# Kernel tuning notes

Hardware: AMD Instinct MI355X
Metric: run time of the kernel (lower is better)

Reference implementation:

```python
import jax, jax.numpy as jnp
import numpy as np

PATCH_SIZE = 8
STRIDE = 4

def setup_inputs() -> dict:
    key = jax.random.key(0)
    k_x, k_w1, k_b1, k_w2, k_b2 = jax.random.split(key, 5)
    B, L, C = 8, 2048, 256
    X = jax.random.normal(k_x, (B, L, C), dtype=jnp.float32)
    # Conv1d(1, 64, patch_size) weight [64,1,ps] -> [64, ps]; Conv1d(64,2,1) -> [2,64]
    s1 = 1.0 / np.sqrt(PATCH_SIZE)
    s2 = 1.0 / np.sqrt(64.0)
    W1 = jax.random.uniform(k_w1, (64, PATCH_SIZE), jnp.float32, -s1, s1)
    b1 = jax.random.uniform(k_b1, (64,), jnp.float32, -s1, s1)
    W2 = jax.random.uniform(k_w2, (2, 64), jnp.float32, -s2, s2)
    b2 = jax.random.uniform(k_b2, (2,), jnp.float32, -s2, s2)
    return {"X": X, "W1": W1, "b1": b1, "W2": W2, "b2": b2}

def reference(X, W1, b1, W2, b2):
    B, L, C = X.shape
    ps, stride = PATCH_SIZE, STRIDE
    patch_count = (L - ps) // stride + 1  # 511
    # gather indices for sliding windows along sequence dim
    idx = jnp.arange(patch_count)[:, None] * stride + jnp.arange(ps)[None, :]  # [pc, ps]
    patches = X[:, idx, :]  # [B, pc, ps, C]
    # per-(patch, channel) MLP: ps -> 64 -> GELU(exact) -> 2
    h = jnp.einsum('bpsc,hs->bpch', patches, W1) + b1  # [B, pc, C, 64]
    h = jax.nn.gelu(h, approximate=False)
    out = jnp.einsum('bpch,oh->bpco', h, W2) + b2  # [B, pc, C, 2]
    return out
```

## Files before the change

### kernel.cpp

```cpp
#include <hip/hip_runtime.h>

#define L_DIM 2048
#define C_DIM 256
#define P_CNT 511
#define H_DIM 64

__device__ __forceinline__ float fast_gelu(float x) {
    float x2 = x * x;
    float t  = x * __builtin_fmaf(x2, -0.0713548162f, -1.5957691216f);
    float e  = __expf(t);
    return x * __builtin_amdgcn_rcpf(1.0f + e);
}

__global__ __launch_bounds__(256, 4) void offset_predictor_kernel(
    const float* __restrict__ X,
    const float* __restrict__ W1,
    const float* __restrict__ b1,
    const float* __restrict__ W2,
    const float* __restrict__ b2,
    float* __restrict__ out)
{
    __shared__ float sWp[H_DIM * 12];
    __shared__ float sB2[2];

    const int tx = threadIdx.x;
    if (tx < H_DIM) {
        float4 wa = *(const float4*)(W1 + tx * 8);
        float4 wb = *(const float4*)(W1 + tx * 8 + 4);
        *(float4*)(sWp + tx * 12)     = wa;
        *(float4*)(sWp + tx * 12 + 4) = wb;
        sWp[tx * 12 + 8]  = b1[tx];
        sWp[tx * 12 + 9]  = W2[tx];
        sWp[tx * 12 + 10] = W2[H_DIM + tx];
        sWp[tx * 12 + 11] = 0.0f;
    }
    if (tx < 2) sB2[tx] = b2[tx];
    __syncthreads();

    const int tid   = blockIdx.x * 256 + tx;
    const int cpair = tid & 127;
    const int ptile = (tid >> 7) & 255;
    const int b     = tid >> 15;
    const int c0    = cpair * 2;
    const int p0    = ptile * 2;

    const float* xb = X + (size_t)b * (L_DIM * C_DIM) + c0;
    float2 xv[12];
#pragma unroll
    for (int j = 0; j < 12; ++j) {
        int l = 4 * p0 + j;
        if (l > L_DIM - 1) l = L_DIM - 1;
        xv[j] = *(const float2*)(xb + (size_t)l * C_DIM);
    }

    const float bo0 = sB2[0], bo1 = sB2[1];
    float4 acc0 = make_float4(bo0, bo1, bo0, bo1);
    float4 acc1 = make_float4(bo0, bo1, bo0, bo1);

#pragma unroll 8
    for (int h = 0; h < H_DIM; ++h) {
        const float4 wa = *(const float4*)(sWp + h * 12);
        const float4 wb = *(const float4*)(sWp + h * 12 + 4);
        const float4 wc = *(const float4*)(sWp + h * 12 + 8);

        float t0 = wc.x, t1 = wc.x;
        float u0 = wc.x, u1 = wc.x;
#define TAP(A0, A1, J, W) \
        A0 = __builtin_fmaf(xv[J].x, (W), A0); \
        A1 = __builtin_fmaf(xv[J].y, (W), A1);
        TAP(t0, t1, 0, wa.x) TAP(t0, t1, 1, wa.y) TAP(t0, t1, 2, wa.z) TAP(t0, t1, 3, wa.w)
        TAP(t0, t1, 4, wb.x) TAP(t0, t1, 5, wb.y) TAP(t0, t1, 6, wb.z) TAP(t0, t1, 7, wb.w)
        TAP(u0, u1, 4, wa.x) TAP(u0, u1, 5, wa.y) TAP(u0, u1, 6, wa.z) TAP(u0, u1, 7, wa.w)
        TAP(u0, u1, 8, wb.x) TAP(u0, u1, 9, wb.y) TAP(u0, u1, 10, wb.z) TAP(u0, u1, 11, wb.w)
#undef TAP
        const float g0 = fast_gelu(t0);
        const float g1 = fast_gelu(t1);
        const float g2 = fast_gelu(u0);
        const float g3 = fast_gelu(u1);
        acc0.x = __builtin_fmaf(g0, wc.y, acc0.x);
        acc0.y = __builtin_fmaf(g0, wc.z, acc0.y);
        acc0.z = __builtin_fmaf(g1, wc.y, acc0.z);
        acc0.w = __builtin_fmaf(g1, wc.z, acc0.w);
        acc1.x = __builtin_fmaf(g2, wc.y, acc1.x);
        acc1.y = __builtin_fmaf(g2, wc.z, acc1.y);
        acc1.z = __builtin_fmaf(g3, wc.y, acc1.z);
        acc1.w = __builtin_fmaf(g3, wc.z, acc1.w);
    }

    float* ob = out + (size_t)b * (P_CNT * C_DIM * 2) + (size_t)c0 * 2;
    *(float4*)(ob + (size_t)p0 * (C_DIM * 2)) = acc0;
    if (p0 + 1 < P_CNT)
        *(float4*)(ob + (size_t)(p0 + 1) * (C_DIM * 2)) = acc1;
}

extern "C" void kernel_launch(void* const* d_in, const int* in_sizes, int n_in,
                              void* d_out, int out_size, void* d_ws, size_t ws_size,
                              hipStream_t stream) {
    const float* X  = (const float*)d_in[0];
    const float* W1 = (const float*)d_in[1];
    const float* b1 = (const float*)d_in[2];
    const float* W2 = (const float*)d_in[3];
    const float* b2 = (const float*)d_in[4];
    float* out = (float*)d_out;

    offset_predictor_kernel<<<1024, 256, 0, stream>>>(X, W1, b1, W2, b2, out);
}
```

Baseline: 104.9 us.

## Use one channel per thread, read weights from global, drop LDS staging

Each thread now handles a single channel instead of a channel pair, so the grid doubles to 2048 blocks and per-thread register use drops. Launch bounds rise to 8 blocks per CU. The shared-memory weight staging and its barrier are removed; weights are read directly from global memory as uniform loads. The aim is higher occupancy and no per-block setup. In exchange, each weight fetch now serves half as much work, so weight-load traffic per FLOP doubles and the X loads become scalar instead of float2.

Result: faster. 101.9 us (-2.8%).

```diff
diff --git a/kernel.cpp b/kernel.cpp
--- a/kernel.cpp
+++ b/kernel.cpp
@@ -12,7 +12,7 @@
     return x * __builtin_amdgcn_rcpf(1.0f + e);
 }
 
-__global__ __launch_bounds__(256, 4) void offset_predictor_kernel(
+__global__ __launch_bounds__(256, 8) void offset_predictor_kernel(
     const float* __restrict__ X,
     const float* __restrict__ W1,
     const float* __restrict__ b1,
@@ -20,77 +20,64 @@
     const float* __restrict__ b2,
     float* __restrict__ out)
 {
-    __shared__ float sWp[H_DIM * 12];
-    __shared__ float sB2[2];
-
-    const int tx = threadIdx.x;
-    if (tx < H_DIM) {
-        float4 wa = *(const float4*)(W1 + tx * 8);
-        float4 wb = *(const float4*)(W1 + tx * 8 + 4);
-        *(float4*)(sWp + tx * 12)     = wa;
-        *(float4*)(sWp + tx * 12 + 4) = wb;
-        sWp[tx * 12 + 8]  = b1[tx];
-        sWp[tx * 12 + 9]  = W2[tx];
-        sWp[tx * 12 + 10] = W2[H_DIM + tx];
-        sWp[tx * 12 + 11] = 0.0f;
-    }
-    if (tx < 2) sB2[tx] = b2[tx];
-    __syncthreads();
-
-    const int tid   = blockIdx.x * 256 + tx;
-    const int cpair = tid & 127;
-    const int ptile = (tid >> 7) & 255;
-    const int b     = tid >> 15;
-    const int c0    = cpair * 2;
+    const int tid   = blockIdx.x * 256 + threadIdx.x;
+    const int c     = tid & 255;
+    const int ptile = (tid >> 8) & 255;
+    const int b     = tid >> 16;
     const int p0    = ptile * 2;
 
-    const float* xb = X + (size_t)b * (L_DIM * C_DIM) + c0;
-    float2 xv[12];
+    const float* xb = X + (size_t)b * (L_DIM * C_DIM) + c;
+    float xv[12];
 #pragma unroll
     for (int j = 0; j < 12; ++j) {
         int l = 4 * p0 + j;
         if (l > L_DIM - 1) l = L_DIM - 1;
-        xv[j] = *(const float2*)(xb + (size_t)l * C_DIM);
+        xv[j] = xb[(size_t)l * C_DIM];
     }
 
-    const float bo0 = sB2[0], bo1 = sB2[1];
-    float4 acc0 = make_float4(bo0, bo1, bo0, bo1);
-    float4 acc1 = make_float4(bo0, bo1, bo0, bo1);
+    const float bo0 = b2[0], bo1 = b2[1];
+    float2 acc0 = make_float2(bo0, bo1);
+    float2 acc1 = make_float2(bo0, bo1);
 
-#pragma unroll 8
+#pragma unroll 4
     for (int h = 0; h < H_DIM; ++h) {
-        const float4 wa = *(const float4*)(sWp + h * 12);
-        const float4 wb = *(const float4*)(sWp + h * 12 + 4);
-        const float4 wc = *(const float4*)(sWp + h * 12 + 8);
+        const float4 wa  = *(const float4*)(W1 + h * 8);
+        const float4 wb  = *(const float4*)(W1 + h * 8 + 4);
+        const float b1h  = b1[h];
+        const float w2a  = W2[h];
+        const float w2b  = W2[H_DIM + h];
 
-        float t0 = wc.x, t1 = wc.x;
-        float u0 = wc.x, u1 = wc.x;
-#define TAP(A0, A1, J, W) \
-        A0 = __builtin_fmaf(xv[J].x, (W), A0); \
-        A1 = __builtin_fmaf(xv[J].y, (W), A1);
-        TAP(t0, t1, 0, wa.x) TAP(t0, t1, 1, wa.y) TAP(t0, t1, 2, wa.z) TAP(t0, t1, 3, wa.w)
-        TAP(t0, t1, 4, wb.x) TAP(t0, t1, 5, wb.y) TAP(t0, t1, 6, wb.z) TAP(t0, t1, 7, wb.w)
-        TAP(u0, u1, 4, wa.x) TAP(u0, u1, 5, wa.y) TAP(u0, u1, 6, wa.z) TAP(u0, u1, 7, wa.w)
-        TAP(u0, u1, 8, wb.x) TAP(u0, u1, 9, wb.y) TAP(u0, u1, 10, wb.z) TAP(u0, u1, 11, wb.w)
-#undef TAP
+        float t0 = b1h;
+        float u0 = b1h;
+        t0 = __builtin_fmaf(xv[0],  wa.x, t0);
+        t0 = __builtin_fmaf(xv[1],  wa.y, t0);
+        t0 = __builtin_fmaf(xv[2],  wa.z, t0);
+        t0 = __builtin_fmaf(xv[3],  wa.w, t0);
+        t0 = __builtin_fmaf(xv[4],  wb.x, t0);
+        t0 = __builtin_fmaf(xv[5],  wb.y, t0);
+        t0 = __builtin_fmaf(xv[6],  wb.z, t0);
+        t0 = __builtin_fmaf(xv[7],  wb.w, t0);
+        u0 = __builtin_fmaf(xv[4],  wa.x, u0);
+        u0 = __builtin_fmaf(xv[5],  wa.y, u0);
+        u0 = __builtin_fmaf(xv[6],  wa.z, u0);
+        u0 = __builtin_fmaf(xv[7],  wa.w, u0);
+        u0 = __builtin_fmaf(xv[8],  wb.x, u0);
+        u0 = __builtin_fmaf(xv[9],  wb.y, u0);
+        u0 = __builtin_fmaf(xv[10], wb.z, u0);
+        u0 = __builtin_fmaf(xv[11], wb.w, u0);
+
         const float g0 = fast_gelu(t0);
-        const float g1 = fast_gelu(t1);
-        const float g2 = fast_gelu(u0);
-        const float g3 = fast_gelu(u1);
-        acc0.x = __builtin_fmaf(g0, wc.y, acc0.x);
-        acc0.y = __builtin_fmaf(g0, wc.z, acc0.y);
-        acc0.z = __builtin_fmaf(g1, wc.y, acc0.z);
-        acc0.w = __builtin_fmaf(g1, wc.z, acc0.w);
-        acc1.x = __builtin_fmaf(g2, wc.y, acc1.x);
-        acc1.y = __builtin_fmaf(g2, wc.z, acc1.y);
-        acc1.z = __builtin_fmaf(g3, wc.y, acc1.z);
-        acc1.w = __builtin_fmaf(g3, wc.z, acc1.w);
+        const float g1 = fast_gelu(u0);
+        acc0.x = __builtin_fmaf(g0, w2a, acc0.x);
+        acc0.y = __builtin_fmaf(g0, w2b, acc0.y);
+        acc1.x = __builtin_fmaf(g1, w2a, acc1.x);
+        acc1.y = __builtin_fmaf(g1, w2b, acc1.y);
     }
 
-    float* ob = out + (size_t)b * (P_CNT * C_DIM * 2) + (size_t)c0 * 2;
-    *(float4*)(ob + (size_t)p0 * (C_DIM * 2)) = acc0;
+    float* ob = out + ((size_t)(b * P_CNT) * C_DIM + c) * 2;
+    *(float2*)(ob + (size_t)p0 * (C_DIM * 2)) = acc0;
     if (p0 + 1 < P_CNT)
-        *(float4*)(ob + (size_t)(p0 + 1) * (C_DIM * 2)) = acc1;
+        *(float2*)(ob + (size_t)(p0 + 1) * (C_DIM * 2)) = acc1;
 }
 
 extern "C" void kernel_launch(void* const* d_in, const int* in_sizes, int n_in,
@@ -103,5 +90,5 @@
     const float* b2 = (const float*)d_in[4];
     float* out = (float*)d_out;
 
-    offset_predictor_kernel<<<1024, 256, 0, stream>>>(X, W1, b1, W2, b2, out);
+    offset_predictor_kernel<<<2048, 256, 0, stream>>>(X, W1, b1, W2, b2, out);
 }
```
